# Optimization experiments

Measured on AMD Instinct MI355X. Metric: run time of the kernel, lower is better.

The kernel has to match this reference:

```python
import jax, jax.numpy as jnp
import numpy as np

V, E, H = 348, 512, 1024  # vocab, embed dim, GRU hidden


def gru_cell(x, h, w_ih, w_hh, b_ih, b_hh):
    # PyTorch GRUCell: gates ordered [r, z, n] along the 3H axis
    gi = x @ w_ih.T + b_ih            # [B, 3H]
    gh = h @ w_hh.T + b_hh            # [B, 3H]
    i_r, i_z, i_n = jnp.split(gi, 3, axis=-1)
    h_r, h_z, h_n = jnp.split(gh, 3, axis=-1)
    r = jax.nn.sigmoid(i_r + h_r)
    z = jax.nn.sigmoid(i_z + h_z)
    n = jnp.tanh(i_n + r * h_n)
    return (1.0 - z) * n + z * h


def setup_inputs() -> dict:
    key = jax.random.key(0)
    ks = jax.random.split(key, 20)
    B, T = 256, 128
    p = lambda k, shape: jax.random.normal(k, shape, dtype=jnp.float32) * 0.02
    return {
        "target": jax.random.randint(ks[0], (B, T), 0, V, dtype=jnp.int32),
        "bos": 1,
        "emb": p(ks[1], (V, E)),
        "w_ih1": p(ks[2], (3 * H, E)),  "w_hh1": p(ks[3], (3 * H, H)),
        "b_ih1": p(ks[4], (3 * H,)),    "b_hh1": p(ks[5], (3 * H,)),
        "w_ih2": p(ks[6], (3 * H, H)),  "w_hh2": p(ks[7], (3 * H, H)),
        "b_ih2": p(ks[8], (3 * H,)),    "b_hh2": p(ks[9], (3 * H,)),
        "w_ih3": p(ks[10], (3 * H, H)), "w_hh3": p(ks[11], (3 * H, H)),
        "b_ih3": p(ks[12], (3 * H,)),   "b_hh3": p(ks[13], (3 * H,)),
        "w_out": p(ks[14], (V, H)),     "b_out": p(ks[15], (V,)),
    }


def reference(target, bos, emb, w_ih1, w_hh1, b_ih1, b_hh1,
              w_ih2, w_hh2, b_ih2, b_hh2,
              w_ih3, w_hh3, b_ih3, b_hh3, w_out, b_out):
    B, T = target.shape
    # input tokens = [<bos>, target[:, :-1]]
    x_in = jnp.concatenate(
        [jnp.full((B, 1), bos, dtype=target.dtype), target[:, :-1]], axis=1)
    h0 = jnp.zeros((B, H), jnp.float32)
    lp0 = jnp.zeros((B,), jnp.float32)

    def step(carry, xt):
        h1, h2, h3, lp = carry
        tok, tgt = xt                     # [B], [B]
        e = emb[tok]                      # [B, E]
        h1 = gru_cell(e, h1, w_ih1, w_hh1, b_ih1, b_hh1)
        h2 = gru_cell(h1, h2, w_ih2, w_hh2, b_ih2, b_hh2)
        h3 = gru_cell(h2, h3, w_ih3, w_hh3, b_ih3, b_hh3)
        logits = h3 @ w_out.T + b_out     # [B, V]
        logp = jax.nn.log_softmax(logits, axis=-1)
        # NLLLoss in source = sum(one_hot(tgt) * log_prob) = gathered log-prob
        lp = lp + jnp.take_along_axis(logp, tgt[:, None], axis=1)[:, 0]
        return (h1, h2, h3, lp), None

    (_, _, _, log_probs), _ = jax.lax.scan(
        step, (h0, h0, h0, lp0), (x_in.T, target.T))
    return log_probs
```

## Files before the change

### kernel.cpp

```cpp
#include <hip/hip_runtime.h>
#include <hip/hip_bf16.h>
#include <cstdint>

constexpr int kT = 128;
constexpr int kB = 256;
constexpr int kE = 512;
constexpr int kH = 1024;
constexpr int kV = 348;
constexpr int kNG = 3072;
constexpr int NB = 208;

constexpr float kScale = 32.f;
constexpr float kInvSS = 1.f / 1024.f;

typedef float f4v __attribute__((ext_vector_type(4)));
typedef unsigned short u16;
typedef unsigned char u8;

__device__ __forceinline__ u8 f2e4m3(float x) {
  int p = __builtin_amdgcn_cvt_pk_fp8_f32(x, x, 0, false);
  return (u8)(p & 0xff);
}

__device__ __forceinline__ uint64_t ldv_u64(const void* p) {
  return __hip_atomic_load((const uint64_t*)p, __ATOMIC_RELAXED, __HIP_MEMORY_SCOPE_AGENT);
}
__device__ __forceinline__ void stv_u8(u8* p, u8 v) {
  __hip_atomic_store(p, v, __ATOMIC_RELAXED, __HIP_MEMORY_SCOPE_AGENT);
}

__device__ __forceinline__ int permn(int n) {
  int gate = n >> 10, j = n & 1023;
  return ((j >> 4) * 48) + gate * 16 + (j & 15);
}

struct Params {
  const int* target; const int* bosp; const float* b_out;
  const u8 *w1i, *w1h, *w2i, *w2h, *w3i, *w3h, *wout, *embb;
  const float *bi1, *bh1, *bi2, *bh2, *bi3, *bh3;
  float *h1f, *h2f, *h3f;
  u8    *h1b, *h2b, *h3b;
  float *lp;
  unsigned *acnt; unsigned *gflag;
};

union SMem {
  struct { u8 A[128 * 144]; u8 B[96 * 144]; } mm;
  float logits[16 * 400];
};

__device__ __forceinline__ void gbar(unsigned* acnt, unsigned* gflag, unsigned s) {
  asm volatile("s_waitcnt vmcnt(0)" ::: "memory");
  __syncthreads();
  if (threadIdx.x == 0) {
    const unsigned g = blockIdx.x & 31u;
    __hip_atomic_fetch_add(&acnt[g * 16], 1u, __ATOMIC_RELAXED, __HIP_MEMORY_SCOPE_AGENT);
    if (blockIdx.x == 0) {
      for (;;) {
        unsigned sum = 0;
#pragma unroll
        for (int i = 0; i < 32; ++i)
          sum += __hip_atomic_load(&acnt[i * 16], __ATOMIC_RELAXED, __HIP_MEMORY_SCOPE_AGENT);
        if (sum >= (unsigned)NB * (s + 1u)) break;
        __builtin_amdgcn_s_sleep(4);
      }
#pragma unroll
      for (int i = 0; i < 32; ++i)
        __hip_atomic_store(&gflag[i * 16], s + 1u, __ATOMIC_RELAXED, __HIP_MEMORY_SCOPE_AGENT);
    } else {
      while (__hip_atomic_load(&gflag[g * 16], __ATOMIC_RELAXED, __HIP_MEMORY_SCOPE_AGENT) <= s)
        __builtin_amdgcn_s_sleep(8);
    }
    asm volatile("" ::: "memory");
  }
  __syncthreads();
}

template<int K, bool EMB>
__device__ __forceinline__ void mm_phase(SMem& sm, const u8* __restrict__ Asrc,
    const u8* __restrict__ W, int b0, int n0,
    f4v* aR, f4v* aZ, f4v* aN,
    const int* __restrict__ target, int bos, int u)
{
  const int t = threadIdx.x, lane = t & 63, wv = t >> 6;
  const int wm = wv >> 1, wg = wv & 1, li = lane & 15, q = lane >> 4;
  uint64_t ra[4][2];
  uint4 rb[3];

  auto stage = [&](int k0) {
#pragma unroll
    for (int p = 0; p < 4; ++p) {
      int id = p * 256 + t, r = id >> 3, c = id & 7;
      if (EMB) {
        int tok = (u == 0) ? bos : target[(b0 + r) * kT + (u - 1)];
        uint4 v = *(const uint4*)&Asrc[(size_t)tok * K + k0 + c * 16];
        ra[p][0] = ((uint64_t)v.y << 32) | v.x;
        ra[p][1] = ((uint64_t)v.w << 32) | v.z;
      } else {
        const u8* src = Asrc + (size_t)(b0 + r) * kH + k0 + c * 16;
        ra[p][0] = ldv_u64(src); ra[p][1] = ldv_u64(src + 8);
      }
    }
#pragma unroll
    for (int p = 0; p < 3; ++p) {
      int id = p * 256 + t, r = id >> 3, c = id & 7;
      rb[p] = *(const uint4*)&W[(size_t)(n0 + r) * K + k0 + c * 16];
    }
  };

  stage(0);
  for (int it = 0; it < K / 128; ++it) {
    __syncthreads();
#pragma unroll
    for (int p = 0; p < 4; ++p) {
      int id = p * 256 + t, r = id >> 3, c = id & 7;
      *(uint64_t*)&sm.mm.A[r * 144 + c * 16] = ra[p][0];
      *(uint64_t*)&sm.mm.A[r * 144 + c * 16 + 8] = ra[p][1];
    }
#pragma unroll
    for (int p = 0; p < 3; ++p) {
      int id = p * 256 + t, r = id >> 3, c = id & 7;
      *(uint4*)&sm.mm.B[r * 144 + c * 16] = rb[p];
    }
    __syncthreads();
    if (it + 1 < K / 128) stage((it + 1) * 128);
#pragma unroll
    for (int kk = 0; kk < 128; kk += 32) {
      int lk = kk + q * 8;
      long a[4], bb[3];
#pragma unroll
      for (int m2 = 0; m2 < 4; ++m2)
        a[m2] = *(const long*)&sm.mm.A[(64 * wm + 16 * m2 + li) * 144 + lk];
#pragma unroll
      for (int g = 0; g < 3; ++g)
        bb[g] = *(const long*)&sm.mm.B[(48 * wg + 16 * g + li) * 144 + lk];
#pragma unroll
      for (int m2 = 0; m2 < 4; ++m2) {
        aR[m2] = __builtin_amdgcn_mfma_f32_16x16x32_fp8_fp8(a[m2], bb[0], aR[m2], 0, 0, 0);
        aZ[m2] = __builtin_amdgcn_mfma_f32_16x16x32_fp8_fp8(a[m2], bb[1], aZ[m2], 0, 0, 0);
        aN[m2] = __builtin_amdgcn_mfma_f32_16x16x32_fp8_fp8(a[m2], bb[2], aN[m2], 0, 0, 0);
      }
    }
  }
}

template<int K1, bool L1>
__device__ void do_L(SMem& sm, const u8* __restrict__ xsrc,
                     const u8* __restrict__ hbPrev, const float* __restrict__ hfPrev,
                     const u8* __restrict__ Wih, const u8* __restrict__ Whh,
                     const float* __restrict__ biP, const float* __restrict__ bhP,
                     float* __restrict__ hfOut, u8* __restrict__ hbOut,
                     const int* __restrict__ target, int bos, int u, int mt, int jt)
{
  const int b0 = mt * 128, j0 = jt * 32, n0 = jt * 96;
  f4v aR[4], aZ[4], aNi[4], aNh[4];
#pragma unroll
  for (int i = 0; i < 4; ++i) {
    aR[i] = f4v{0.f,0.f,0.f,0.f}; aZ[i] = f4v{0.f,0.f,0.f,0.f};
    aNi[i] = f4v{0.f,0.f,0.f,0.f}; aNh[i] = f4v{0.f,0.f,0.f,0.f};
  }
  mm_phase<K1, L1>(sm, xsrc, Wih, b0, n0, aR, aZ, aNi, target, bos, u);
  mm_phase<kH, false>(sm, hbPrev, Whh, b0, n0, aR, aZ, aNh, target, bos, u);

  const int t = threadIdx.x, lane = t & 63, wv = t >> 6;
  const int wm = wv >> 1, wg = wv & 1, li = lane & 15, q = lane >> 4;
  const int j = j0 + 16 * wg + li;
  const int cr = n0 + 48 * wg + li;
  const float bR = biP[cr] + bhP[cr];
  const float bZ = biP[cr + 16] + bhP[cr + 16];
  const float biN = biP[cr + 32], bhN = bhP[cr + 32];
  float hold[4][4];
#pragma unroll
  for (int m2 = 0; m2 < 4; ++m2)
#pragma unroll
    for (int r = 0; r < 4; ++r) {
      int b = b0 + 64 * wm + 16 * m2 + 4 * q + r;
      hold[m2][r] = hfPrev[(size_t)b * kH + j];
    }
#pragma unroll
  for (int m2 = 0; m2 < 4; ++m2)
#pragma unroll
    for (int r = 0; r < 4; ++r) {
      int b = b0 + 64 * wm + 16 * m2 + 4 * q + r;
      float rg = 1.f / (1.f + __expf(-(aR[m2][r] * kInvSS + bR)));
      float zg = 1.f / (1.f + __expf(-(aZ[m2][r] * kInvSS + bZ)));
      float np = (aNi[m2][r] * kInvSS + biN) + rg * (aNh[m2][r] * kInvSS + bhN);
      float nh = 2.f / (1.f + __expf(-2.f * np)) - 1.f;
      float hnew = (1.f - zg) * nh + zg * hold[m2][r];
      hfOut[(size_t)b * kH + j] = hnew;
      stv_u8(&hbOut[(size_t)b * kH + j], f2e4m3(hnew * kScale));
    }
}

__device__ void do_E(SMem& sm, const u8* __restrict__ h3b, const u8* __restrict__ wo,
                     const float* __restrict__ b_out, const int* __restrict__ target,
                     float* __restrict__ lp, int u, int tile)
{
  const int b0 = tile * 16;
  const int t = threadIdx.x, lane = t & 63, wv = t >> 6;
  const int li = lane & 15, q = lane >> 4;
  f4v acc[6];
#pragma unroll
  for (int f = 0; f < 6; ++f) acc[f] = f4v{0.f, 0.f, 0.f, 0.f};

  const u8* ap = h3b + (size_t)(b0 + li) * kH + q * 8;
  uint64_t aCur = ldv_u64(ap);
  uint64_t bCur[6], bNx[6];
#pragma unroll
  for (int f = 0; f < 6; ++f)
    bCur[f] = *(const uint64_t*)&wo[(size_t)(96 * wv + 16 * f + li) * kH + q * 8];
  for (int k0 = 0; k0 < kH; k0 += 32) {
    uint64_t aNx = 0;
    if (k0 + 32 < kH) {
      aNx = ldv_u64(ap + k0 + 32);
#pragma unroll
      for (int f = 0; f < 6; ++f)
        bNx[f] = *(const uint64_t*)&wo[(size_t)(96 * wv + 16 * f + li) * kH + k0 + 32 + q * 8];
    }
#pragma unroll
    for (int f = 0; f < 6; ++f)
      acc[f] = __builtin_amdgcn_mfma_f32_16x16x32_fp8_fp8((long)aCur, (long)bCur[f], acc[f], 0, 0, 0);
    aCur = aNx;
#pragma unroll
    for (int f = 0; f < 6; ++f) bCur[f] = bNx[f];
  }
#pragma unroll
  for (int f = 0; f < 6; ++f) {
    int n = 96 * wv + 16 * f + li;
    if (n < kV) {
      float bo = b_out[n];
#pragma unroll
      for (int r = 0; r < 4; ++r)
        sm.logits[(4 * q + r) * 400 + n] = acc[f][r] * kInvSS + bo;
    }
  }
  __syncthreads();
  int m = 4 * wv + q;
  int b = b0 + m;
  float mx = -1e30f;
  for (int cc = li; cc < kV; cc += 16) mx = fmaxf(mx, sm.logits[m * 400 + cc]);
#pragma unroll
  for (int d = 1; d < 16; d <<= 1) mx = fmaxf(mx, __shfl_xor(mx, d, 16));
  float se = 0.f;
  for (int cc = li; cc < kV; cc += 16) se += __expf(sm.logits[m * 400 + cc] - mx);
#pragma unroll
  for (int d = 1; d < 16; d <<= 1) se += __shfl_xor(se, d, 16);
  int tgt = target[b * kT + u];
  float logp = sm.logits[m * 400 + tgt] - mx - __logf(se);
  if (li == 0) lp[b] += logp;
}

__global__ __launch_bounds__(256, 1) void rnn_main(Params P)
{
  __shared__ SMem sm;
  const int bid = blockIdx.x;
  const int bos = P.bosp[0];
  const size_t HS = (size_t)kB * kH;

  const int local = bid & 63;
  const int mt = (local >> 3) & 1;
  const int jt = (local & 7) | ((local >> 4) << 3);

  for (int s = 0; s < kT + 3; ++s) {
    if (bid < 64) {
      int u = s;
      if (u < kT)
        do_L<kE, true>(sm, P.embb,
                       P.h1b + (size_t)((u - 1) & 1) * HS, P.h1f + (size_t)((u - 1) & 1) * HS,
                       P.w1i, P.w1h, P.bi1, P.bh1,
                       P.h1f + (size_t)(u & 1) * HS, P.h1b + (size_t)(u & 1) * HS,
                       P.target, bos, u, mt, jt);
    } else if (bid < 128) {
      int u = s - 1;
      if (u >= 0 && u < kT)
        do_L<kH, false>(sm, P.h1b + (size_t)(u & 1) * HS,
                        P.h2b + (size_t)((u - 1) & 1) * HS, P.h2f + (size_t)((u - 1) & 1) * HS,
                        P.w2i, P.w2h, P.bi2, P.bh2,
                        P.h2f + (size_t)(u & 1) * HS, P.h2b + (size_t)(u & 1) * HS,
                        P.target, bos, u, mt, jt);
    } else if (bid < 192) {
      int u = s - 2;
      if (u >= 0 && u < kT)
        do_L<kH, false>(sm, P.h2b + (size_t)(u & 1) * HS,
                        P.h3b + (size_t)((u - 1) & 1) * HS, P.h3f + (size_t)((u - 1) & 1) * HS,
                        P.w3i, P.w3h, P.bi3, P.bh3,
                        P.h3f + (size_t)(u & 1) * HS, P.h3b + (size_t)(u & 1) * HS,
                        P.target, bos, u, mt, jt);
    } else {
      int u = s - 3;
      if (u >= 0 && u < kT)
        do_E(sm, P.h3b + (size_t)(u & 1) * HS, P.wout, P.b_out, P.target, P.lp, u, bid - 192);
    }
    gbar(P.acnt, P.gflag, (unsigned)s);
  }
}

__global__ void k_conv_w(const float* __restrict__ w, u8* __restrict__ wp, int K, int logK) {
  int idx = blockIdx.x * 256 + threadIdx.x;
  if (idx >= kNG * K) return;
  int n = idx >> logK, k = idx & (K - 1);
  wp[(size_t)permn(n) * K + k] = f2e4m3(w[idx] * kScale);
}
__global__ void k_conv_b(const float* __restrict__ b, float* __restrict__ bp) {
  int idx = blockIdx.x * 256 + threadIdx.x;
  if (idx < kNG) bp[permn(idx)] = b[idx];
}
__global__ void k_conv_wout(const float* __restrict__ w, u8* __restrict__ wp) {
  int idx = blockIdx.x * 256 + threadIdx.x;
  if (idx >= 384 * kH) return;
  int n = idx >> 10, k = idx & 1023;
  wp[idx] = (n < kV) ? f2e4m3(w[(size_t)n * kH + k] * kScale) : (u8)0;
}
__global__ void k_conv_emb(const float* __restrict__ e, u8* __restrict__ ep) {
  int idx = blockIdx.x * 256 + threadIdx.x;
  if (idx < kV * kE) ep[idx] = f2e4m3(e[idx] * kScale);
}

extern "C" void kernel_launch(void* const* d_in, const int* in_sizes, int n_in,
                              void* d_out, int out_size, void* d_ws, size_t ws_size,
                              hipStream_t stream)
{
  const int*   target = (const int*)d_in[0];
  const int*   bosp   = (const int*)d_in[1];
  const float* emb    = (const float*)d_in[2];
  const float* w_ih1  = (const float*)d_in[3];
  const float* w_hh1  = (const float*)d_in[4];
  const float* b_ih1  = (const float*)d_in[5];
  const float* b_hh1  = (const float*)d_in[6];
  const float* w_ih2  = (const float*)d_in[7];
  const float* w_hh2  = (const float*)d_in[8];
  const float* b_ih2  = (const float*)d_in[9];
  const float* b_hh2  = (const float*)d_in[10];
  const float* w_ih3  = (const float*)d_in[11];
  const float* w_hh3  = (const float*)d_in[12];
  const float* b_ih3  = (const float*)d_in[13];
  const float* b_hh3  = (const float*)d_in[14];
  const float* w_out  = (const float*)d_in[15];
  const float* b_out  = (const float*)d_in[16];

  char* ws = (char*)d_ws;
  size_t off = 0;
  auto alloc = [&](size_t bytes) -> void* {
    void* p = ws + off;
    off = (off + bytes + 511) & ~(size_t)511;
    return p;
  };
  u8* w1i = (u8*)alloc((size_t)kNG * kE);
  u8* w1h = (u8*)alloc((size_t)kNG * kH);
  u8* w2i = (u8*)alloc((size_t)kNG * kH);
  u8* w2h = (u8*)alloc((size_t)kNG * kH);
  u8* w3i = (u8*)alloc((size_t)kNG * kH);
  u8* w3h = (u8*)alloc((size_t)kNG * kH);
  u8* wo  = (u8*)alloc((size_t)384 * kH);
  u8* eb  = (u8*)alloc((size_t)kV * kE);
  float* bi1 = (float*)alloc(kNG * 4);
  float* bh1 = (float*)alloc(kNG * 4);
  float* bi2 = (float*)alloc(kNG * 4);
  float* bh2 = (float*)alloc(kNG * 4);
  float* bi3 = (float*)alloc(kNG * 4);
  float* bh3 = (float*)alloc(kNG * 4);
  float* h1f = (float*)alloc((size_t)2 * kB * kH * 4);
  float* h2f = (float*)alloc((size_t)2 * kB * kH * 4);
  float* h3f = (float*)alloc((size_t)2 * kB * kH * 4);
  u8* h1b = (u8*)alloc((size_t)2 * kB * kH);
  u8* h2b = (u8*)alloc((size_t)2 * kB * kH);
  u8* h3b = (u8*)alloc((size_t)2 * kB * kH);
  unsigned* bar = (unsigned*)alloc(4096);
  (void)ws_size; (void)in_sizes; (void)n_in; (void)out_size;

  k_conv_w<<<(kNG * kE + 255) / 256, 256, 0, stream>>>(w_ih1, w1i, kE, 9);
  k_conv_w<<<(kNG * kH + 255) / 256, 256, 0, stream>>>(w_hh1, w1h, kH, 10);
  k_conv_w<<<(kNG * kH + 255) / 256, 256, 0, stream>>>(w_ih2, w2i, kH, 10);
  k_conv_w<<<(kNG * kH + 255) / 256, 256, 0, stream>>>(w_hh2, w2h, kH, 10);
  k_conv_w<<<(kNG * kH + 255) / 256, 256, 0, stream>>>(w_ih3, w3i, kH, 10);
  k_conv_w<<<(kNG * kH + 255) / 256, 256, 0, stream>>>(w_hh3, w3h, kH, 10);
  k_conv_b<<<(kNG + 255) / 256, 256, 0, stream>>>(b_ih1, bi1);
  k_conv_b<<<(kNG + 255) / 256, 256, 0, stream>>>(b_hh1, bh1);
  k_conv_b<<<(kNG + 255) / 256, 256, 0, stream>>>(b_ih2, bi2);
  k_conv_b<<<(kNG + 255) / 256, 256, 0, stream>>>(b_hh2, bh2);
  k_conv_b<<<(kNG + 255) / 256, 256, 0, stream>>>(b_ih3, bi3);
  k_conv_b<<<(kNG + 255) / 256, 256, 0, stream>>>(b_hh3, bh3);
  k_conv_wout<<<(384 * kH + 255) / 256, 256, 0, stream>>>(w_out, wo);
  k_conv_emb<<<(kV * kE + 255) / 256, 256, 0, stream>>>(emb, eb);

  hipMemsetAsync(h1f, 0, (size_t)3 * 2 * kB * kH * 4, stream);
  hipMemsetAsync(h1b, 0, (size_t)3 * 2 * kB * kH, stream);
  hipMemsetAsync(bar, 0, 4096, stream);
  hipMemsetAsync(d_out, 0, (size_t)kB * 4, stream);

  Params P;
  P.target = target; P.bosp = bosp; P.b_out = b_out;
  P.w1i = w1i; P.w1h = w1h; P.w2i = w2i; P.w2h = w2h; P.w3i = w3i; P.w3h = w3h;
  P.wout = wo; P.embb = eb;
  P.bi1 = bi1; P.bh1 = bh1; P.bi2 = bi2; P.bh2 = bh2; P.bi3 = bi3; P.bh3 = bh3;
  P.h1f = h1f; P.h2f = h2f; P.h3f = h3f;
  P.h1b = h1b; P.h2b = h2b; P.h3b = h3b;
  P.lp = (float*)d_out;
  P.acnt = bar; P.gflag = bar + 512;

  rnn_main<<<dim3(NB), dim3(256), 0, stream>>>(P);
}
```

Measured before the change: 4.543 ms.

## Double-buffer LDS tiles and fuse input/hidden GEMM phases into one pipelined loop

The two separate mm_phase calls are merged into one loop over all K tiles of the input and hidden GEMMs. Shared memory is double-buffered, so the writes for the next tile overlap the MFMAs on the current one and each tile needs one barrier instead of two. The output-projection routine now preloads the whole A row strip into 32 registers and fully unrolls the K loop. The cost is more LDS and higher register pressure, which could lower occupancy or cause spills.

```diff
diff --git a/kernel.cpp b/kernel.cpp
--- a/kernel.cpp
+++ b/kernel.cpp
@@ -45,7 +45,7 @@
 };
 
 union SMem {
-  struct { u8 A[128 * 144]; u8 B[96 * 144]; } mm;
+  struct { u8 A[2][128 * 144]; u8 B[2][96 * 144]; } mm;
   float logits[16 * 400];
 };
 
@@ -76,75 +76,7 @@
   __syncthreads();
 }
 
-template<int K, bool EMB>
-__device__ __forceinline__ void mm_phase(SMem& sm, const u8* __restrict__ Asrc,
-    const u8* __restrict__ W, int b0, int n0,
-    f4v* aR, f4v* aZ, f4v* aN,
-    const int* __restrict__ target, int bos, int u)
-{
-  const int t = threadIdx.x, lane = t & 63, wv = t >> 6;
-  const int wm = wv >> 1, wg = wv & 1, li = lane & 15, q = lane >> 4;
-  uint64_t ra[4][2];
-  uint4 rb[3];
-
-  auto stage = [&](int k0) {
-#pragma unroll
-    for (int p = 0; p < 4; ++p) {
-      int id = p * 256 + t, r = id >> 3, c = id & 7;
-      if (EMB) {
-        int tok = (u == 0) ? bos : target[(b0 + r) * kT + (u - 1)];
-        uint4 v = *(const uint4*)&Asrc[(size_t)tok * K + k0 + c * 16];
-        ra[p][0] = ((uint64_t)v.y << 32) | v.x;
-        ra[p][1] = ((uint64_t)v.w << 32) | v.z;
-      } else {
-        const u8* src = Asrc + (size_t)(b0 + r) * kH + k0 + c * 16;
-        ra[p][0] = ldv_u64(src); ra[p][1] = ldv_u64(src + 8);
-      }
-    }
-#pragma unroll
-    for (int p = 0; p < 3; ++p) {
-      int id = p * 256 + t, r = id >> 3, c = id & 7;
-      rb[p] = *(const uint4*)&W[(size_t)(n0 + r) * K + k0 + c * 16];
-    }
-  };
-
-  stage(0);
-  for (int it = 0; it < K / 128; ++it) {
-    __syncthreads();
-#pragma unroll
-    for (int p = 0; p < 4; ++p) {
-      int id = p * 256 + t, r = id >> 3, c = id & 7;
-      *(uint64_t*)&sm.mm.A[r * 144 + c * 16] = ra[p][0];
-      *(uint64_t*)&sm.mm.A[r * 144 + c * 16 + 8] = ra[p][1];
-    }
-#pragma unroll
-    for (int p = 0; p < 3; ++p) {
-      int id = p * 256 + t, r = id >> 3, c = id & 7;
-      *(uint4*)&sm.mm.B[r * 144 + c * 16] = rb[p];
-    }
-    __syncthreads();
-    if (it + 1 < K / 128) stage((it + 1) * 128);
-#pragma unroll
-    for (int kk = 0; kk < 128; kk += 32) {
-      int lk = kk + q * 8;
-      long a[4], bb[3];
-#pragma unroll
-      for (int m2 = 0; m2 < 4; ++m2)
-        a[m2] = *(const long*)&sm.mm.A[(64 * wm + 16 * m2 + li) * 144 + lk];
-#pragma unroll
-      for (int g = 0; g < 3; ++g)
-        bb[g] = *(const long*)&sm.mm.B[(48 * wg + 16 * g + li) * 144 + lk];
-#pragma unroll
-      for (int m2 = 0; m2 < 4; ++m2) {
-        aR[m2] = __builtin_amdgcn_mfma_f32_16x16x32_fp8_fp8(a[m2], bb[0], aR[m2], 0, 0, 0);
-        aZ[m2] = __builtin_amdgcn_mfma_f32_16x16x32_fp8_fp8(a[m2], bb[1], aZ[m2], 0, 0, 0);
-        aN[m2] = __builtin_amdgcn_mfma_f32_16x16x32_fp8_fp8(a[m2], bb[2], aN[m2], 0, 0, 0);
-      }
-    }
-  }
-}
-
-template<int K1, bool L1>
+template<int K1, bool EMB>
 __device__ void do_L(SMem& sm, const u8* __restrict__ xsrc,
                      const u8* __restrict__ hbPrev, const float* __restrict__ hfPrev,
                      const u8* __restrict__ Wih, const u8* __restrict__ Whh,
@@ -152,18 +84,100 @@
                      float* __restrict__ hfOut, u8* __restrict__ hbOut,
                      const int* __restrict__ target, int bos, int u, int mt, int jt)
 {
+  constexpr int T1 = K1 / 128;
+  constexpr int NT = T1 + kH / 128;
   const int b0 = mt * 128, j0 = jt * 32, n0 = jt * 96;
+  const int t = threadIdx.x, lane = t & 63, wv = t >> 6;
+  const int wm = wv >> 1, wg = wv & 1, li = lane & 15, q = lane >> 4;
+
   f4v aR[4], aZ[4], aNi[4], aNh[4];
 #pragma unroll
   for (int i = 0; i < 4; ++i) {
     aR[i] = f4v{0.f,0.f,0.f,0.f}; aZ[i] = f4v{0.f,0.f,0.f,0.f};
     aNi[i] = f4v{0.f,0.f,0.f,0.f}; aNh[i] = f4v{0.f,0.f,0.f,0.f};
   }
-  mm_phase<K1, L1>(sm, xsrc, Wih, b0, n0, aR, aZ, aNi, target, bos, u);
-  mm_phase<kH, false>(sm, hbPrev, Whh, b0, n0, aR, aZ, aNh, target, bos, u);
-
-  const int t = threadIdx.x, lane = t & 63, wv = t >> 6;
-  const int wm = wv >> 1, wg = wv & 1, li = lane & 15, q = lane >> 4;
+
+  int rA[4], cA[4], tokp[4];
+#pragma unroll
+  for (int p = 0; p < 4; ++p) {
+    int id = p * 256 + t; rA[p] = id >> 3; cA[p] = (id & 7) * 16;
+    if (EMB) tokp[p] = (u == 0) ? bos : target[(b0 + rA[p]) * kT + (u - 1)];
+  }
+  int rB[3], cB[3];
+#pragma unroll
+  for (int p = 0; p < 3; ++p) { int id = p * 256 + t; rB[p] = id >> 3; cB[p] = (id & 7) * 16; }
+
+  uint64_t ra0[4][2], ra1[4][2];
+  uint4 rb0[3], rb1[3];
+
+  auto stage = [&](int tt, uint64_t (&ra)[4][2], uint4 (&rb)[3]) {
+    const bool gi = tt < T1;
+    const int k0 = (gi ? tt : tt - T1) * 128;
+#pragma unroll
+    for (int p = 0; p < 4; ++p) {
+      if (gi && EMB) {
+        uint4 v = *(const uint4*)&xsrc[(size_t)tokp[p] * K1 + k0 + cA[p]];
+        ra[p][0] = ((uint64_t)v.y << 32) | v.x;
+        ra[p][1] = ((uint64_t)v.w << 32) | v.z;
+      } else {
+        const u8* src = (gi ? xsrc : hbPrev) + (size_t)(b0 + rA[p]) * kH + k0 + cA[p];
+        ra[p][0] = ldv_u64(src); ra[p][1] = ldv_u64(src + 8);
+      }
+    }
+#pragma unroll
+    for (int p = 0; p < 3; ++p)
+      rb[p] = gi ? *(const uint4*)&Wih[(size_t)(n0 + rB[p]) * K1 + k0 + cB[p]]
+                 : *(const uint4*)&Whh[(size_t)(n0 + rB[p]) * kH + k0 + cB[p]];
+  };
+
+  auto wr = [&](int bi, uint64_t (&ra)[4][2], uint4 (&rb)[3]) {
+#pragma unroll
+    for (int p = 0; p < 4; ++p) {
+      *(uint64_t*)&sm.mm.A[bi][rA[p] * 144 + cA[p]] = ra[p][0];
+      *(uint64_t*)&sm.mm.A[bi][rA[p] * 144 + cA[p] + 8] = ra[p][1];
+    }
+#pragma unroll
+    for (int p = 0; p < 3; ++p)
+      *(uint4*)&sm.mm.B[bi][rB[p] * 144 + cB[p]] = rb[p];
+  };
+
+  auto mfma_on = [&](int bi, f4v (&aN)[4]) {
+#pragma unroll
+    for (int kk = 0; kk < 128; kk += 32) {
+      const int lk = kk + q * 8;
+      long a[4], bb[3];
+#pragma unroll
+      for (int m2 = 0; m2 < 4; ++m2)
+        a[m2] = *(const long*)&sm.mm.A[bi][(64 * wm + 16 * m2 + li) * 144 + lk];
+#pragma unroll
+      for (int g = 0; g < 3; ++g)
+        bb[g] = *(const long*)&sm.mm.B[bi][(48 * wg + 16 * g + li) * 144 + lk];
+#pragma unroll
+      for (int m2 = 0; m2 < 4; ++m2) {
+        aR[m2] = __builtin_amdgcn_mfma_f32_16x16x32_fp8_fp8(a[m2], bb[0], aR[m2], 0, 0, 0);
+        aZ[m2] = __builtin_amdgcn_mfma_f32_16x16x32_fp8_fp8(a[m2], bb[1], aZ[m2], 0, 0, 0);
+        aN[m2] = __builtin_amdgcn_mfma_f32_16x16x32_fp8_fp8(a[m2], bb[2], aN[m2], 0, 0, 0);
+      }
+    }
+  };
+
+  stage(0, ra0, rb0);
+  stage(1, ra1, rb1);
+  wr(0, ra0, rb0);
+  __syncthreads();
+
+#pragma unroll 1
+  for (int tt = 0; tt < NT; tt += 2) {
+    if (tt + 2 < NT) stage(tt + 2, ra0, rb0);
+    if (tt < T1) mfma_on(0, aNi); else mfma_on(0, aNh);
+    wr(1, ra1, rb1);
+    __syncthreads();
+    if (tt + 3 < NT) stage(tt + 3, ra1, rb1);
+    if (tt + 1 < T1) mfma_on(1, aNi); else mfma_on(1, aNh);
+    if (tt + 2 < NT) wr(0, ra0, rb0);
+    __syncthreads();
+  }
+
   const int j = j0 + 16 * wg + li;
   const int cr = n0 + 48 * wg + li;
   const float bR = biP[cr] + bhP[cr];
@@ -204,25 +218,29 @@
   for (int f = 0; f < 6; ++f) acc[f] = f4v{0.f, 0.f, 0.f, 0.f};
 
   const u8* ap = h3b + (size_t)(b0 + li) * kH + q * 8;
-  uint64_t aCur = ldv_u64(ap);
-  uint64_t bCur[6], bNx[6];
-#pragma unroll
-  for (int f = 0; f < 6; ++f)
-    bCur[f] = *(const uint64_t*)&wo[(size_t)(96 * wv + 16 * f + li) * kH + q * 8];
-  for (int k0 = 0; k0 < kH; k0 += 32) {
-    uint64_t aNx = 0;
-    if (k0 + 32 < kH) {
-      aNx = ldv_u64(ap + k0 + 32);
+  uint64_t aAll[32];
+#pragma unroll
+  for (int k = 0; k < 32; ++k) aAll[k] = ldv_u64(ap + k * 32);
+
+  const u8* wp = wo + (size_t)(96 * wv + li) * kH + q * 8;
+  uint64_t bC[6];
+#pragma unroll
+  for (int f = 0; f < 6; ++f) bC[f] = *(const uint64_t*)(wp + (size_t)16 * f * kH);
+#pragma unroll
+  for (int k0 = 0; k0 < 32; ++k0) {
+    uint64_t bN[6];
+    if (k0 + 1 < 32) {
 #pragma unroll
       for (int f = 0; f < 6; ++f)
-        bNx[f] = *(const uint64_t*)&wo[(size_t)(96 * wv + 16 * f + li) * kH + k0 + 32 + q * 8];
+        bN[f] = *(const uint64_t*)(wp + (size_t)16 * f * kH + (k0 + 1) * 32);
     }
 #pragma unroll
     for (int f = 0; f < 6; ++f)
-      acc[f] = __builtin_amdgcn_mfma_f32_16x16x32_fp8_fp8((long)aCur, (long)bCur[f], acc[f], 0, 0, 0);
-    aCur = aNx;
-#pragma unroll
-    for (int f = 0; f < 6; ++f) bCur[f] = bNx[f];
+      acc[f] = __builtin_amdgcn_mfma_f32_16x16x32_fp8_fp8((long)aAll[k0], (long)bC[f], acc[f], 0, 0, 0);
+    if (k0 + 1 < 32) {
+#pragma unroll
+      for (int f = 0; f < 6; ++f) bC[f] = bN[f];
+    }
   }
 #pragma unroll
   for (int f = 0; f < 6; ++f) {
```

Result: slower. 10.53 ms (+131.8%).

## Double-buffer A-tile register prefetch and XOR-swizzle LDS tiles in fp8 GEMM

Applied to the files above, without the earlier changes.

The fp8 MFMA main loop now prefetches A-operand tiles two steps ahead using even/odd register buffers, so global loads are in flight longer before they are needed. The padded 144-byte LDS row stride is replaced by a dense 128-byte stride with an XOR swizzle on 8-byte chunks, which shrinks LDS usage while aiming to avoid bank conflicts. The cost is more live registers, which may reduce occupancy or cause spills. The loop assumes K/128 is even, which holds for K=512 and K=1024.

```diff
diff --git a/kernel.cpp b/kernel.cpp
--- a/kernel.cpp
+++ b/kernel.cpp
@@ -45,7 +45,7 @@
 };
 
 union SMem {
-  struct { u8 A[128 * 144]; u8 B[96 * 144]; } mm;
+  struct { u8 A[128 * 128]; u8 B[96 * 128]; } mm;
   float logits[16 * 400];
 };
 
@@ -76,6 +76,65 @@
   __syncthreads();
 }
 
+#define LOAD_A(dst, k0)                                                      \
+  _Pragma("unroll")                                                          \
+  for (int p = 0; p < 4; ++p) {                                              \
+    int id = p * 256 + t, r = id >> 3, c = id & 7;                           \
+    if (EMB) {                                                               \
+      int tok = (u == 0) ? bos : target[(b0 + r) * kT + (u - 1)];            \
+      uint4 v = *(const uint4*)&Asrc[(size_t)tok * K + (k0) + c * 16];       \
+      dst[p][0] = ((uint64_t)v.y << 32) | v.x;                               \
+      dst[p][1] = ((uint64_t)v.w << 32) | v.z;                               \
+    } else {                                                                 \
+      const u8* srcp = Asrc + (size_t)(b0 + r) * kH + (k0) + c * 16;         \
+      dst[p][0] = ldv_u64(srcp); dst[p][1] = ldv_u64(srcp + 8);              \
+    }                                                                        \
+  }
+
+#define LOAD_B(k0)                                                           \
+  _Pragma("unroll")                                                          \
+  for (int p = 0; p < 3; ++p) {                                              \
+    int id = p * 256 + t, r = id >> 3, c = id & 7;                           \
+    rb[p] = *(const uint4*)&W[(size_t)(n0 + r) * K + (k0) + c * 16];         \
+  }
+
+#define WR_AB(srcA)                                                          \
+  _Pragma("unroll")                                                          \
+  for (int p = 0; p < 4; ++p) {                                              \
+    int id = p * 256 + t, r = id >> 3, c = id & 7;                           \
+    const int u0 = c * 2, rx = r & 15;                                       \
+    u8* base = &sm.mm.A[r * 128];                                            \
+    *(uint64_t*)(base + 8 * (u0 ^ rx)) = srcA[p][0];                         \
+    *(uint64_t*)(base + 8 * ((u0 + 1) ^ rx)) = srcA[p][1];                   \
+  }                                                                          \
+  _Pragma("unroll")                                                          \
+  for (int p = 0; p < 3; ++p) {                                              \
+    int id = p * 256 + t, r = id >> 3, c = id & 7;                           \
+    const int u0 = c * 2, rx = r & 15;                                       \
+    u8* base = &sm.mm.B[r * 128];                                            \
+    *(uint64_t*)(base + 8 * (u0 ^ rx)) = (uint64_t)rb[p].x | ((uint64_t)rb[p].y << 32); \
+    *(uint64_t*)(base + 8 * ((u0 + 1) ^ rx)) = (uint64_t)rb[p].z | ((uint64_t)rb[p].w << 32); \
+  }
+
+#define MFMA_TILE()                                                          \
+  _Pragma("unroll")                                                          \
+  for (int kk = 0; kk < 128; kk += 32) {                                     \
+    const int swz = 8 * (((kk >> 3) + q) ^ li);                              \
+    long a[4], bb[3];                                                        \
+    _Pragma("unroll")                                                        \
+    for (int m2 = 0; m2 < 4; ++m2)                                           \
+      a[m2] = *(const long*)&sm.mm.A[(64 * wm + 16 * m2 + li) * 128 + swz];  \
+    _Pragma("unroll")                                                        \
+    for (int g = 0; g < 3; ++g)                                              \
+      bb[g] = *(const long*)&sm.mm.B[(48 * wg + 16 * g + li) * 128 + swz];   \
+    _Pragma("unroll")                                                        \
+    for (int m2 = 0; m2 < 4; ++m2) {                                         \
+      aR[m2] = __builtin_amdgcn_mfma_f32_16x16x32_fp8_fp8(a[m2], bb[0], aR[m2], 0, 0, 0); \
+      aZ[m2] = __builtin_amdgcn_mfma_f32_16x16x32_fp8_fp8(a[m2], bb[1], aZ[m2], 0, 0, 0); \
+      aN[m2] = __builtin_amdgcn_mfma_f32_16x16x32_fp8_fp8(a[m2], bb[2], aN[m2], 0, 0, 0); \
+    }                                                                        \
+  }
+
 template<int K, bool EMB>
 __device__ __forceinline__ void mm_phase(SMem& sm, const u8* __restrict__ Asrc,
     const u8* __restrict__ W, int b0, int n0,
@@ -84,63 +143,28 @@
 {
   const int t = threadIdx.x, lane = t & 63, wv = t >> 6;
   const int wm = wv >> 1, wg = wv & 1, li = lane & 15, q = lane >> 4;
-  uint64_t ra[4][2];
+  constexpr int NT = K / 128;
+  uint64_t raE[4][2], raO[4][2];
   uint4 rb[3];
 
-  auto stage = [&](int k0) {
-#pragma unroll
-    for (int p = 0; p < 4; ++p) {
-      int id = p * 256 + t, r = id >> 3, c = id & 7;
-      if (EMB) {
-        int tok = (u == 0) ? bos : target[(b0 + r) * kT + (u - 1)];
-        uint4 v = *(const uint4*)&Asrc[(size_t)tok * K + k0 + c * 16];
-        ra[p][0] = ((uint64_t)v.y << 32) | v.x;
-        ra[p][1] = ((uint64_t)v.w << 32) | v.z;
-      } else {
-        const u8* src = Asrc + (size_t)(b0 + r) * kH + k0 + c * 16;
-        ra[p][0] = ldv_u64(src); ra[p][1] = ldv_u64(src + 8);
-      }
-    }
-#pragma unroll
-    for (int p = 0; p < 3; ++p) {
-      int id = p * 256 + t, r = id >> 3, c = id & 7;
-      rb[p] = *(const uint4*)&W[(size_t)(n0 + r) * K + k0 + c * 16];
-    }
-  };
-
-  stage(0);
-  for (int it = 0; it < K / 128; ++it) {
+  LOAD_A(raE, 0)
+  LOAD_A(raO, 128)
+  LOAD_B(0)
+
+#pragma unroll 1
+  for (int it = 0; it < NT; it += 2) {
     __syncthreads();
-#pragma unroll
-    for (int p = 0; p < 4; ++p) {
-      int id = p * 256 + t, r = id >> 3, c = id & 7;
-      *(uint64_t*)&sm.mm.A[r * 144 + c * 16] = ra[p][0];
-      *(uint64_t*)&sm.mm.A[r * 144 + c * 16 + 8] = ra[p][1];
-    }
-#pragma unroll
-    for (int p = 0; p < 3; ++p) {
-      int id = p * 256 + t, r = id >> 3, c = id & 7;
-      *(uint4*)&sm.mm.B[r * 144 + c * 16] = rb[p];
-    }
+    WR_AB(raE)
     __syncthreads();
-    if (it + 1 < K / 128) stage((it + 1) * 128);
-#pragma unroll
-    for (int kk = 0; kk < 128; kk += 32) {
-      int lk = kk + q * 8;
-      long a[4], bb[3];
-#pragma unroll
-      for (int m2 = 0; m2 < 4; ++m2)
-        a[m2] = *(const long*)&sm.mm.A[(64 * wm + 16 * m2 + li) * 144 + lk];
-#pragma unroll
-      for (int g = 0; g < 3; ++g)
-        bb[g] = *(const long*)&sm.mm.B[(48 * wg + 16 * g + li) * 144 + lk];
-#pragma unroll
-      for (int m2 = 0; m2 < 4; ++m2) {
-        aR[m2] = __builtin_amdgcn_mfma_f32_16x16x32_fp8_fp8(a[m2], bb[0], aR[m2], 0, 0, 0);
-        aZ[m2] = __builtin_amdgcn_mfma_f32_16x16x32_fp8_fp8(a[m2], bb[1], aZ[m2], 0, 0, 0);
-        aN[m2] = __builtin_amdgcn_mfma_f32_16x16x32_fp8_fp8(a[m2], bb[2], aN[m2], 0, 0, 0);
-      }
-    }
+    if (it + 2 < NT) { LOAD_A(raE, (it + 2) * 128) }
+    LOAD_B((it + 1) * 128)
+    MFMA_TILE()
+    __syncthreads();
+    WR_AB(raO)
+    __syncthreads();
+    if (it + 3 < NT) { LOAD_A(raO, (it + 3) * 128) }
+    if (it + 2 < NT) { LOAD_B((it + 2) * 128) }
+    MFMA_TILE()
   }
 }
 
```

Measured after the change: 4.000 ms. 12.0% less time.
